# Optimization experiments

Measured on AMD Instinct MI355X. Metric: run time of the kernel, lower is better.

The kernel has to match this reference:

```python
import jax, jax.numpy as jnp
import numpy as np

ALPHA = 0.2  # LeakyReLU negative slope
NEG_INF = -9e15


def setup_inputs() -> dict:
    key = jax.random.key(0)
    k1, k2, k3, k4 = jax.random.split(key, 4)
    N, C, T, V, F = 64, 64, 300, 25, 64
    x = jax.random.normal(k1, (N, C, T, V), dtype=jnp.float32)
    adj = jax.random.randint(k2, (V, V), 0, 2, dtype=jnp.int32)
    # Xavier-uniform-like scale for params
    W = jax.random.normal(k3, (C, F), dtype=jnp.float32) * 0.15
    a = jax.random.normal(k4, (2 * F, 1), dtype=jnp.float32) * 0.1
    return {"x": x, "adj": adj, "W": W, "a": a}


def reference(x, adj, W, a):
    # x: (N, C, T, V), adj: (V, V), W: (C, F), a: (2F, 1)
    Fdim = W.shape[1]
    # h = permute+view+matmul of original, kept in (N, T, V, F) layout
    h = jnp.einsum('nctv,cf->ntvf', x, W)
    # Additive attention: cat([h_i, h_j]) @ a == h_i @ a1 + h_j @ a2
    a1 = a[:Fdim, 0]   # (F,)
    a2 = a[Fdim:, 0]   # (F,)
    f1 = h @ a1        # (N, T, V)
    f2 = h @ a2        # (N, T, V)
    e = jax.nn.leaky_relu(f1[..., :, None] + f2[..., None, :], ALPHA)  # (N,T,V,V)
    e = jnp.where(adj > 0, e, NEG_INF)
    att = jax.nn.softmax(e, axis=-1)
    # dropout omitted (eval mode / deterministic reference)
    h_prime = jnp.einsum('ntij,ntjf->ntif', att, h)  # (N, T, V, F)
    h_prime = jax.nn.elu(h_prime)                    # concat=True branch
    return jnp.transpose(h_prime, (0, 3, 1, 2))      # (N, F, T, V)
```

## Files before the change

### kernel.cpp

```cpp
#include <hip/hip_runtime.h>
#include <math.h>

constexpr int Nn = 64, Cc = 64, Tt = 300, Vv = 25, Ff = 64;
constexpr int TP = Tt / 2;
constexpr int VP = 28;
constexpr int HS = 68;
constexpr float ALPHA = 0.2f;
constexpr float NEG_INF = -9.0e15f;

__global__ __launch_bounds__(256, 3) void gat_kernel(
    const float* __restrict__ x,
    const int*   __restrict__ adj,
    const float* __restrict__ W,
    const float* __restrict__ a,
    float* __restrict__ out)
{
    __shared__ float Ws[Cc][Ff];
    __shared__ float xs_hp[2][Cc][VP];
    __shared__ float hs[2][VP][HS];
    __shared__ float attT[2][Vv][VP];
    __shared__ float f1s[2][Vv], f2s[2][Vv];
    __shared__ float a1s[Ff], a2s[Ff];
    __shared__ unsigned adjm[Vv];

    const int tid = threadIdx.x;
    const int blk = blockIdx.x;
    const int n = blk / TP, tp = blk - n * TP;
    const int t0 = tp * 2;

    {
        const float4* W4 = (const float4*)W;
        float4* Ws4 = (float4*)&Ws[0][0];
        #pragma unroll
        for (int i = 0; i < 4; ++i) Ws4[i * 256 + tid] = W4[i * 256 + tid];
    }
    {
        const float* xb = x + (size_t)n * Cc * Tt * Vv + (size_t)t0 * Vv;
        const int j = tid & 63, cg = tid >> 6;
        const int pp = (j >= Vv) ? 1 : 0;
        const int v  = j - Vv * pp;
        if (j < 2 * Vv) {
            #pragma unroll
            for (int i = 0; i < 16; ++i) {
                int c = i * 4 + cg;
                xs_hp[pp][c][v] = xb[(size_t)c * (Tt * Vv) + j];
            }
        }
    }
    if (tid < Ff) { a1s[tid] = a[tid]; a2s[tid] = a[Ff + tid]; }
    else if (tid >= 128 && tid < 128 + Vv) {
        int i = tid - 128; unsigned m = 0;
        for (int j = 0; j < Vv; ++j) m |= (adj[i * Vv + j] > 0 ? 1u : 0u) << j;
        adjm[i] = m;
    }
    __syncthreads();

    const int p  = tid >> 7;
    const int l  = tid & 127;
    const int f4 = l & 15;
    const int vg = l >> 4;
    const int v0 = vg * 4;

    if (vg < 7) {
        float4 acc0{0,0,0,0}, acc1{0,0,0,0}, acc2{0,0,0,0}, acc3{0,0,0,0};
        for (int c = 0; c < Cc; ++c) {
            const float4 w  = *(const float4*)&Ws[c][f4 * 4];
            const float4 xv = *(const float4*)&xs_hp[p][c][v0];
            acc0.x += xv.x * w.x; acc0.y += xv.x * w.y; acc0.z += xv.x * w.z; acc0.w += xv.x * w.w;
            acc1.x += xv.y * w.x; acc1.y += xv.y * w.y; acc1.z += xv.y * w.z; acc1.w += xv.y * w.w;
            acc2.x += xv.z * w.x; acc2.y += xv.z * w.y; acc2.z += xv.z * w.z; acc2.w += xv.z * w.w;
            acc3.x += xv.w * w.x; acc3.y += xv.w * w.y; acc3.z += xv.w * w.z; acc3.w += xv.w * w.w;
        }
        *(float4*)&hs[p][v0 + 0][f4 * 4] = acc0;
        *(float4*)&hs[p][v0 + 1][f4 * 4] = acc1;
        *(float4*)&hs[p][v0 + 2][f4 * 4] = acc2;
        *(float4*)&hs[p][v0 + 3][f4 * 4] = acc3;
    }
    __syncthreads();

    if (l < 2 * Vv) {
        const int i = (l < Vv) ? l : l - Vv;
        const float* av = (l < Vv) ? a1s : a2s;
        float s = 0.f;
        #pragma unroll
        for (int q = 0; q < Ff / 4; ++q) {
            float4 h4 = *(const float4*)&hs[p][i][q * 4];
            float4 a4 = *(const float4*)&av[q * 4];
            s += h4.x * a4.x + h4.y * a4.y + h4.z * a4.z + h4.w * a4.w;
        }
        if (l < Vv) f1s[p][i] = s; else f2s[p][i] = s;
    }
    __syncthreads();

    if (l < Vv) {
        const int i = l;
        const float fi = f1s[p][i];
        const unsigned m = adjm[i];
        float ev[Vv];
        float mx = -INFINITY;
        #pragma unroll
        for (int j = 0; j < Vv; ++j) {
            float z = fi + f2s[p][j];
            z = (z > 0.f) ? z : ALPHA * z;
            z = ((m >> j) & 1u) ? z : NEG_INF;
            ev[j] = z; mx = fmaxf(mx, z);
        }
        float s = 0.f;
        #pragma unroll
        for (int j = 0; j < Vv; ++j) { float e = __expf(ev[j] - mx); ev[j] = e; s += e; }
        const float inv = 1.f / s;
        #pragma unroll
        for (int j = 0; j < Vv; ++j) attT[p][j][i] = ev[j] * inv;
    }
    __syncthreads();

    if (vg < 7) {
        const int i0 = v0;
        float4 acc[4] = {};
        for (int j = 0; j < Vv; ++j) {
            const float4 at = *(const float4*)&attT[p][j][i0];
            const float4 hv = *(const float4*)&hs[p][j][f4 * 4];
            acc[0].x += hv.x * at.x; acc[0].y += hv.x * at.y; acc[0].z += hv.x * at.z; acc[0].w += hv.x * at.w;
            acc[1].x += hv.y * at.x; acc[1].y += hv.y * at.y; acc[1].z += hv.y * at.z; acc[1].w += hv.y * at.w;
            acc[2].x += hv.z * at.x; acc[2].y += hv.z * at.y; acc[2].z += hv.z * at.z; acc[2].w += hv.z * at.w;
            acc[3].x += hv.w * at.x; acc[3].y += hv.w * at.y; acc[3].z += hv.w * at.z; acc[3].w += hv.w * at.w;
        }
        #pragma unroll
        for (int kf = 0; kf < 4; ++kf) {
            float4 v = acc[kf];
            v.x = (v.x > 0.f) ? v.x : (__expf(v.x) - 1.f);
            v.y = (v.y > 0.f) ? v.y : (__expf(v.y) - 1.f);
            v.z = (v.z > 0.f) ? v.z : (__expf(v.z) - 1.f);
            v.w = (v.w > 0.f) ? v.w : (__expf(v.w) - 1.f);
            *(float4*)&xs_hp[p][f4 * 4 + kf][i0] = v;
        }
    }
    __syncthreads();

    {
        const int i  = tid & 31;
        const int fr = tid >> 5;
        if (i < Vv) {
            #pragma unroll
            for (int pp = 0; pp < 2; ++pp) {
                float* ob = out + ((size_t)n * Ff * Tt + (size_t)(t0 + pp)) * Vv;
                #pragma unroll
                for (int fb = 0; fb < 8; ++fb) {
                    int f = fb * 8 + fr;
                    ob[(size_t)f * Tt * Vv + i] = xs_hp[pp][f][i];
                }
            }
        }
    }
}

extern "C" void kernel_launch(void* const* d_in, const int* in_sizes, int n_in,
                              void* d_out, int out_size, void* d_ws, size_t ws_size,
                              hipStream_t stream) {
    const float* x   = (const float*)d_in[0];
    const int*   adj = (const int*)d_in[1];
    const float* W   = (const float*)d_in[2];
    const float* a   = (const float*)d_in[3];
    float* out = (float*)d_out;

    dim3 grid(Nn * TP);
    dim3 block(256);
    gat_kernel<<<grid, block, 0, stream>>>(x, adj, W, a, out);
}
```

Measured before the change: 303.7 us.

## Remap threads to wave-uniform feature slices with scalar W loads and fused attention scores

Each wave now owns 16 output features, and each lane owns one (time, node) pair. W is read straight from global memory with wave-uniform addresses (readfirstlane), so it can go through scalar loads, and the shared W copy is removed. The f1/f2 attention scores are built from per-wave partial dot products, which drops one sync stage, and f2 is passed between lanes with shuffles. The output is written directly from registers without staging through shared memory. Shared memory shrinks and occupancy is raised to 4 blocks. The cost is that lanes 25-31 of each half-wave do padded work, and W is loaded once per block from global/L2.

```diff
diff --git a/kernel.cpp b/kernel.cpp
--- a/kernel.cpp
+++ b/kernel.cpp
@@ -3,24 +3,20 @@
 
 constexpr int Nn = 64, Cc = 64, Tt = 300, Vv = 25, Ff = 64;
 constexpr int TP = Tt / 2;
-constexpr int VP = 28;
-constexpr int HS = 68;
 constexpr float ALPHA = 0.2f;
 constexpr float NEG_INF = -9.0e15f;
 
-__global__ __launch_bounds__(256, 3) void gat_kernel(
+__global__ __launch_bounds__(256, 4) void gat_kernel(
     const float* __restrict__ x,
     const int*   __restrict__ adj,
     const float* __restrict__ W,
     const float* __restrict__ a,
     float* __restrict__ out)
 {
-    __shared__ float Ws[Cc][Ff];
-    __shared__ float xs_hp[2][Cc][VP];
-    __shared__ float hs[2][VP][HS];
-    __shared__ float attT[2][Vv][VP];
-    __shared__ float f1s[2][Vv], f2s[2][Vv];
-    __shared__ float a1s[Ff], a2s[Ff];
+    __shared__ float xs[2][Cc][32];
+    __shared__ float hs[2][Vv][68];
+    __shared__ float attT[2][Vv][32];
+    __shared__ float fpart[2][4][32][2];
     __shared__ unsigned adjm[Vv];
 
     const int tid = threadIdx.x;
@@ -29,127 +25,122 @@
     const int t0 = tp * 2;
 
     {
-        const float4* W4 = (const float4*)W;
-        float4* Ws4 = (float4*)&Ws[0][0];
-        #pragma unroll
-        for (int i = 0; i < 4; ++i) Ws4[i * 256 + tid] = W4[i * 256 + tid];
-    }
-    {
         const float* xb = x + (size_t)n * Cc * Tt * Vv + (size_t)t0 * Vv;
         const int j = tid & 63, cg = tid >> 6;
         const int pp = (j >= Vv) ? 1 : 0;
-        const int v  = j - Vv * pp;
+        const int vj = j - Vv * pp;
         if (j < 2 * Vv) {
             #pragma unroll
             for (int i = 0; i < 16; ++i) {
-                int c = i * 4 + cg;
-                xs_hp[pp][c][v] = xb[(size_t)c * (Tt * Vv) + j];
+                const int c = i * 4 + cg;
+                xs[pp][c][vj] = xb[(size_t)c * (Tt * Vv) + j];
             }
         }
     }
-    if (tid < Ff) { a1s[tid] = a[tid]; a2s[tid] = a[Ff + tid]; }
-    else if (tid >= 128 && tid < 128 + Vv) {
-        int i = tid - 128; unsigned m = 0;
+    if (tid >= 128 && tid < 128 + Vv) {
+        const int i = tid - 128;
+        unsigned m = 0;
+        #pragma unroll
         for (int j = 0; j < Vv; ++j) m |= (adj[i * Vv + j] > 0 ? 1u : 0u) << j;
         adjm[i] = m;
     }
     __syncthreads();
 
-    const int p  = tid >> 7;
-    const int l  = tid & 127;
-    const int f4 = l & 15;
-    const int vg = l >> 4;
-    const int v0 = vg * 4;
+    const int wid  = tid >> 6;
+    const int lane = tid & 63;
+    const int ph   = lane >> 5;
+    const int v    = lane & 31;
+    const int f0   = __builtin_amdgcn_readfirstlane(wid << 4);
 
-    if (vg < 7) {
-        float4 acc0{0,0,0,0}, acc1{0,0,0,0}, acc2{0,0,0,0}, acc3{0,0,0,0};
-        for (int c = 0; c < Cc; ++c) {
-            const float4 w  = *(const float4*)&Ws[c][f4 * 4];
-            const float4 xv = *(const float4*)&xs_hp[p][c][v0];
-            acc0.x += xv.x * w.x; acc0.y += xv.x * w.y; acc0.z += xv.x * w.z; acc0.w += xv.x * w.w;
-            acc1.x += xv.y * w.x; acc1.y += xv.y * w.y; acc1.z += xv.y * w.z; acc1.w += xv.y * w.w;
-            acc2.x += xv.z * w.x; acc2.y += xv.z * w.y; acc2.z += xv.z * w.z; acc2.w += xv.z * w.w;
-            acc3.x += xv.w * w.x; acc3.y += xv.w * w.y; acc3.z += xv.w * w.z; acc3.w += xv.w * w.w;
+    float acc[16];
+    #pragma unroll
+    for (int k = 0; k < 16; ++k) acc[k] = 0.f;
+
+    const float* __restrict__ Wg = W + f0;
+    const float* xcol = &xs[ph][0][v];
+    #pragma unroll 4
+    for (int c = 0; c < Cc; ++c) {
+        const float xv = xcol[c * 32];
+        float wv[16];
+        *(float4*)&wv[0]  = *(const float4*)(Wg + c * Ff + 0);
+        *(float4*)&wv[4]  = *(const float4*)(Wg + c * Ff + 4);
+        *(float4*)&wv[8]  = *(const float4*)(Wg + c * Ff + 8);
+        *(float4*)&wv[12] = *(const float4*)(Wg + c * Ff + 12);
+        #pragma unroll
+        for (int k = 0; k < 16; ++k) acc[k] += xv * wv[k];
+    }
+
+    float p1 = 0.f, p2 = 0.f;
+    #pragma unroll
+    for (int k = 0; k < 16; ++k) {
+        p1 += acc[k] * a[f0 + k];
+        p2 += acc[k] * a[Ff + f0 + k];
+    }
+
+    if (v < Vv) {
+        #pragma unroll
+        for (int q = 0; q < 4; ++q) {
+            float4 t4;
+            t4.x = acc[q * 4 + 0]; t4.y = acc[q * 4 + 1];
+            t4.z = acc[q * 4 + 2]; t4.w = acc[q * 4 + 3];
+            *(float4*)&hs[ph][v][f0 + q * 4] = t4;
         }
-        *(float4*)&hs[p][v0 + 0][f4 * 4] = acc0;
-        *(float4*)&hs[p][v0 + 1][f4 * 4] = acc1;
-        *(float4*)&hs[p][v0 + 2][f4 * 4] = acc2;
-        *(float4*)&hs[p][v0 + 3][f4 * 4] = acc3;
+        *(float2*)&fpart[ph][wid][v][0] = make_float2(p1, p2);
     }
     __syncthreads();
 
-    if (l < 2 * Vv) {
-        const int i = (l < Vv) ? l : l - Vv;
-        const float* av = (l < Vv) ? a1s : a2s;
-        float s = 0.f;
+    if (tid < 2 * Vv) {
+        const int dp = (tid >= Vv) ? 1 : 0;
+        const int i = tid - Vv * dp;
+        float f1 = 0.f, f2 = 0.f;
         #pragma unroll
-        for (int q = 0; q < Ff / 4; ++q) {
-            float4 h4 = *(const float4*)&hs[p][i][q * 4];
-            float4 a4 = *(const float4*)&av[q * 4];
-            s += h4.x * a4.x + h4.y * a4.y + h4.z * a4.z + h4.w * a4.w;
+        for (int w = 0; w < 4; ++w) {
+            const float2 fp = *(const float2*)&fpart[dp][w][i][0];
+            f1 += fp.x; f2 += fp.y;
         }
-        if (l < Vv) f1s[p][i] = s; else f2s[p][i] = s;
-    }
-    __syncthreads();
-
-    if (l < Vv) {
-        const int i = l;
-        const float fi = f1s[p][i];
         const unsigned m = adjm[i];
         float ev[Vv];
         float mx = -INFINITY;
         #pragma unroll
         for (int j = 0; j < Vv; ++j) {
-            float z = fi + f2s[p][j];
+            const float f2j = __shfl(f2, dp * Vv + j, 64);
+            float z = f1 + f2j;
             z = (z > 0.f) ? z : ALPHA * z;
             z = ((m >> j) & 1u) ? z : NEG_INF;
             ev[j] = z; mx = fmaxf(mx, z);
         }
         float s = 0.f;
         #pragma unroll
-        for (int j = 0; j < Vv; ++j) { float e = __expf(ev[j] - mx); ev[j] = e; s += e; }
+        for (int j = 0; j < Vv; ++j) { const float e = __expf(ev[j] - mx); ev[j] = e; s += e; }
         const float inv = 1.f / s;
         #pragma unroll
-        for (int j = 0; j < Vv; ++j) attT[p][j][i] = ev[j] * inv;
+        for (int j = 0; j < Vv; ++j) attT[dp][j][i] = ev[j] * inv;
     }
     __syncthreads();
 
-    if (vg < 7) {
-        const int i0 = v0;
-        float4 acc[4] = {};
-        for (int j = 0; j < Vv; ++j) {
-            const float4 at = *(const float4*)&attT[p][j][i0];
-            const float4 hv = *(const float4*)&hs[p][j][f4 * 4];
-            acc[0].x += hv.x * at.x; acc[0].y += hv.x * at.y; acc[0].z += hv.x * at.z; acc[0].w += hv.x * at.w;
-            acc[1].x += hv.y * at.x; acc[1].y += hv.y * at.y; acc[1].z += hv.y * at.z; acc[1].w += hv.y * at.w;
-            acc[2].x += hv.z * at.x; acc[2].y += hv.z * at.y; acc[2].z += hv.z * at.z; acc[2].w += hv.z * at.w;
-            acc[3].x += hv.w * at.x; acc[3].y += hv.w * at.y; acc[3].z += hv.w * at.z; acc[3].w += hv.w * at.w;
-        }
+    float acc2[16];
+    #pragma unroll
+    for (int k = 0; k < 16; ++k) acc2[k] = 0.f;
+    const float* attb = &attT[ph][0][v];
+    #pragma unroll 5
+    for (int j = 0; j < Vv; ++j) {
+        const float av = attb[j * 32];
+        float hv[16];
+        *(float4*)&hv[0]  = *(const float4*)&hs[ph][j][f0 + 0];
+        *(float4*)&hv[4]  = *(const float4*)&hs[ph][j][f0 + 4];
+        *(float4*)&hv[8]  = *(const float4*)&hs[ph][j][f0 + 8];
+        *(float4*)&hv[12] = *(const float4*)&hs[ph][j][f0 + 12];
         #pragma unroll
-        for (int kf = 0; kf < 4; ++kf) {
-            float4 v = acc[kf];
-            v.x = (v.x > 0.f) ? v.x : (__expf(v.x) - 1.f);
-            v.y = (v.y > 0.f) ? v.y : (__expf(v.y) - 1.f);
-            v.z = (v.z > 0.f) ? v.z : (__expf(v.z) - 1.f);
-            v.w = (v.w > 0.f) ? v.w : (__expf(v.w) - 1.f);
-            *(float4*)&xs_hp[p][f4 * 4 + kf][i0] = v;
-        }
+        for (int k = 0; k < 16; ++k) acc2[k] += av * hv[k];
     }
-    __syncthreads();
 
-    {
-        const int i  = tid & 31;
-        const int fr = tid >> 5;
-        if (i < Vv) {
-            #pragma unroll
-            for (int pp = 0; pp < 2; ++pp) {
-                float* ob = out + ((size_t)n * Ff * Tt + (size_t)(t0 + pp)) * Vv;
-                #pragma unroll
-                for (int fb = 0; fb < 8; ++fb) {
-                    int f = fb * 8 + fr;
-                    ob[(size_t)f * Tt * Vv + i] = xs_hp[pp][f][i];
-                }
-            }
+    if (v < Vv) {
+        float* ob = out + ((size_t)(n * Ff + f0) * Tt + (size_t)(t0 + ph)) * Vv + v;
+        #pragma unroll
+        for (int k = 0; k < 16; ++k) {
+            float z = acc2[k];
+            z = (z > 0.f) ? z : (__expf(z) - 1.f);
+            ob[(size_t)k * Tt * Vv] = z;
         }
     }
 }
```

After: 291.0 us. 4.2% less time.
